# Kernel tuning notes

Hardware: AMD Instinct MI355X
Metric: run time of the kernel (lower is better)

The kernel has to match this reference:

```python
import jax, jax.numpy as jnp
import numpy as np

B = 1024          # batch
L = 200           # max_len (history length)
DIM = 64          # args.dim
ITEM_NUM = 100000 # vocab; table has ITEM_NUM+1 rows, row 0 = padding
NEG = -1e15       # mask additive constant used by the original module


def setup_inputs() -> dict:
    key = jax.random.key(0)
    k1, k2, k3, k4, k5 = jax.random.split(key, 5)
    log_seqs = jax.random.randint(k1, (B, L), 0, ITEM_NUM + 1)          # item ids, 0 = pad
    pred = jax.random.randint(k2, (B, 1), 0, ITEM_NUM + 1)              # gather targets
    item_emb = jax.random.normal(k3, (ITEM_NUM + 1, DIM), jnp.float32) * 0.02
    item_emb = item_emb.at[0].set(0.0)                                  # padding_idx=0
    attn_key = jax.random.uniform(k4, (1, DIM), jnp.float32)            # self.key (torch.rand init)
    pos_emb = jax.random.normal(k5, (L, DIM), jnp.float32) * 0.02       # positional table
    return {"log_seqs": log_seqs, "pred": pred, "item_emb": item_emb,
            "attn_key": attn_key, "pos_emb": pos_emb}


def reference(log_seqs, pred, item_emb, attn_key, pos_emb):
    dim = item_emb.shape[1]
    mask = log_seqs != 0                                  # [B, L] True where valid
    # log2feats (model='P2MAMO', dropout p=0 -> identity)
    seqs = item_emb[log_seqs] * jnp.sqrt(jnp.float32(dim))  # [B, L, D]
    seqs = seqs + pos_emb[None, :, :]
    seqs = seqs * mask[..., None]                         # zero out padded positions
    # single-query dot-product attention pooling with learned key
    sim = jnp.einsum('bld,d->bl', seqs, attn_key[0])      # (q*k).sum(-1)
    sim = sim + jnp.where(mask, 0.0, NEG)                 # sim + (~mask)*-1e15
    attn = jax.nn.softmax(sim, axis=-1)                   # [B, L]
    Q = jnp.einsum('bld,bl->bd', seqs, attn)              # [B, D]
    # training path (isEval=False): full-vocab logits -> softmax -> gather
    logits = Q @ item_emb.T                               # [B, V+1]
    probs = jax.nn.softmax(logits, axis=-1)
    pos_logits = jnp.take_along_axis(probs, pred, axis=1) # [B, 1]
    return pos_logits
```

## Files before the change

kernel.cpp:

```cpp
#include <hip/hip_runtime.h>
#include <math.h>

#define B_TOT   1024
#define L_SEQ   200
#define DIM     64
#define VOCAB   100001
#define NEG_BIG (-1e15f)
#define SEQ_STRIDE 68

typedef __bf16 bf16x8 __attribute__((ext_vector_type(8)));
typedef float  f32x4  __attribute__((ext_vector_type(4)));

__global__ __launch_bounds__(256) void pool_kernel(
    const int*   __restrict__ log_seqs,
    const float* __restrict__ item_emb,
    const float* __restrict__ attn_key,
    const float* __restrict__ pos_emb,
    float*       __restrict__ Q,
    __bf16*      __restrict__ Qb,
    __bf16*      __restrict__ Eb)
{
    const int b    = blockIdx.x;
    const int t    = threadIdx.x;
    const int wave = t >> 6;
    const int lane = t & 63;

    __shared__ float s_seq[L_SEQ][SEQ_STRIDE];
    __shared__ float s_attn[L_SEQ];
    __shared__ float s_red[4];
    __shared__ float s_q[4][DIM];

    {
        const long n8 = ((long)VOCAB * DIM) / 8;
        for (long g = (long)b * 256 + t; g < n8; g += (long)gridDim.x * 256) {
            const long i = g * 8;
            const float4 f0 = ((const float4*)(item_emb + i))[0];
            const float4 f1 = ((const float4*)(item_emb + i))[1];
            bf16x8 o;
            o[0] = (__bf16)f0.x; o[1] = (__bf16)f0.y; o[2] = (__bf16)f0.z; o[3] = (__bf16)f0.w;
            o[4] = (__bf16)f1.x; o[5] = (__bf16)f1.y; o[6] = (__bf16)f1.z; o[7] = (__bf16)f1.w;
            *(bf16x8*)(Eb + i) = o;
        }
    }

    float sim = -INFINITY;
    if (t < L_SEQ) {
        const int id = log_seqs[(long)b * L_SEQ + t];
        if (id == 0) {
            sim = NEG_BIG;
            #pragma unroll
            for (int i = 0; i < DIM / 4; ++i)
                *(float4*)(&s_seq[t][4 * i]) = make_float4(0.f, 0.f, 0.f, 0.f);
        } else {
            float acc = 0.f;
            const float4* e4 = (const float4*)(item_emb + (long)id * DIM);
            const float4* p4 = (const float4*)(pos_emb + t * DIM);
            #pragma unroll
            for (int i = 0; i < DIM / 4; ++i) {
                const float4 e = e4[i];
                const float4 p = p4[i];
                float4 f;
                f.x = fmaf(8.f, e.x, p.x);
                f.y = fmaf(8.f, e.y, p.y);
                f.z = fmaf(8.f, e.z, p.z);
                f.w = fmaf(8.f, e.w, p.w);
                *(float4*)(&s_seq[t][4 * i]) = f;
                acc += f.x * attn_key[4*i+0] + f.y * attn_key[4*i+1]
                     + f.z * attn_key[4*i+2] + f.w * attn_key[4*i+3];
            }
            sim = acc;
        }
    }

    float m = sim;
    #pragma unroll
    for (int off = 32; off > 0; off >>= 1) m = fmaxf(m, __shfl_xor(m, off));
    if (lane == 0) s_red[wave] = m;
    __syncthreads();
    m = fmaxf(fmaxf(s_red[0], s_red[1]), fmaxf(s_red[2], s_red[3]));
    __syncthreads();

    float p = (t < L_SEQ) ? __expf(sim - m) : 0.f;
    if (t < L_SEQ) s_attn[t] = p;
    float ls = p;
    #pragma unroll
    for (int off = 32; off > 0; off >>= 1) ls += __shfl_xor(ls, off);
    if (lane == 0) s_red[wave] = ls;
    __syncthreads();
    const float inv = 1.0f / (s_red[0] + s_red[1] + s_red[2] + s_red[3]);

    float q = 0.f;
    const int l0 = wave * (L_SEQ / 4);
    #pragma unroll 2
    for (int l = l0; l < l0 + (L_SEQ / 4); ++l)
        q = fmaf(s_attn[l], s_seq[l][lane], q);
    s_q[wave][lane] = q;
    __syncthreads();

    if (t < DIM) {
        const float qq = (s_q[0][t] + s_q[1][t] + s_q[2][t] + s_q[3][t]) * inv;
        Q[b * DIM + t]  = qq;
        Qb[b * DIM + t] = (__bf16)qq;
    }
}

#define NC        128
#define NBG       8
#define VT_TOTAL  6251
#define VT_FULL   6250

__global__ __launch_bounds__(256) void logits_mfma(
    const __bf16* __restrict__ Eb,
    const __bf16* __restrict__ Qb,
    float*        __restrict__ partials)
{
    const int bid   = blockIdx.x;
    const int xcd   = bid & 7;
    const int idx   = bid >> 3;
    const int chunk = xcd + 8 * (idx >> 3);
    const int bg    = idx & 7;
    const int wave  = threadIdx.x >> 6;
    const int lane  = threadIdx.x & 63;
    const int r16   = lane & 15;
    const int hi    = lane >> 4;

    __shared__ float s_part[4][128];

    bf16x8 a[8][2];
    #pragma unroll
    for (int t = 0; t < 8; ++t)
        #pragma unroll
        for (int s = 0; s < 2; ++s)
            a[t][s] = *(const bf16x8*)(Qb + ((bg*128 + t*16 + r16) * DIM) + s*32 + hi*8);

    const int per    = (VT_TOTAL + NC - 1) / NC;
    const int vt_end = min((chunk + 1) * per, VT_TOTAL);
    int vt = chunk * per + wave;

    float ssum[8][4];
    #pragma unroll
    for (int t = 0; t < 8; ++t)
        #pragma unroll
        for (int r = 0; r < 4; ++r) ssum[t][r] = 0.f;

    #define LOADB(dst0, dst1, vti) do {                                       \
        const int _row = min((vti) * 16 + r16, VOCAB - 1);                    \
        const __bf16* _p = Eb + (size_t)_row * DIM + hi * 8;                  \
        dst0 = *(const bf16x8*)_p;                                            \
        dst1 = *(const bf16x8*)(_p + 32);                                     \
    } while (0)

    bf16x8 b0, b1, d0, d1;
    LOADB(b0, b1, vt);
    LOADB(d0, d1, vt + 4);

    while (vt < vt_end) {
        const bf16x8 c00 = b0, c01 = b1, c10 = d0, c11 = d1;
        const int v0 = vt, v1 = vt + 4;
        vt += 8;
        LOADB(b0, b1, vt);
        LOADB(d0, d1, vt + 4);

        if (v0 < VT_FULL) {
            #pragma unroll
            for (int t = 0; t < 8; ++t) {
                f32x4 acc = {0.f, 0.f, 0.f, 0.f};
                acc = __builtin_amdgcn_mfma_f32_16x16x32_bf16(a[t][0], c00, acc, 0, 0, 0);
                acc = __builtin_amdgcn_mfma_f32_16x16x32_bf16(a[t][1], c01, acc, 0, 0, 0);
                #pragma unroll
                for (int r = 0; r < 4; ++r) ssum[t][r] += __expf(acc[r]);
            }
        } else {
            const bool valid = (v0 * 16 + r16) < VOCAB;
            #pragma unroll
            for (int t = 0; t < 8; ++t) {
                f32x4 acc = {0.f, 0.f, 0.f, 0.f};
                acc = __builtin_amdgcn_mfma_f32_16x16x32_bf16(a[t][0], c00, acc, 0, 0, 0);
                acc = __builtin_amdgcn_mfma_f32_16x16x32_bf16(a[t][1], c01, acc, 0, 0, 0);
                #pragma unroll
                for (int r = 0; r < 4; ++r) ssum[t][r] += valid ? __expf(acc[r]) : 0.f;
            }
        }
        if (v1 < vt_end) {
            if (v1 < VT_FULL) {
                #pragma unroll
                for (int t = 0; t < 8; ++t) {
                    f32x4 acc = {0.f, 0.f, 0.f, 0.f};
                    acc = __builtin_amdgcn_mfma_f32_16x16x32_bf16(a[t][0], c10, acc, 0, 0, 0);
                    acc = __builtin_amdgcn_mfma_f32_16x16x32_bf16(a[t][1], c11, acc, 0, 0, 0);
                    #pragma unroll
                    for (int r = 0; r < 4; ++r) ssum[t][r] += __expf(acc[r]);
                }
            } else {
                const bool valid = (v1 * 16 + r16) < VOCAB;
                #pragma unroll
                for (int t = 0; t < 8; ++t) {
                    f32x4 acc = {0.f, 0.f, 0.f, 0.f};
                    acc = __builtin_amdgcn_mfma_f32_16x16x32_bf16(a[t][0], c10, acc, 0, 0, 0);
                    acc = __builtin_amdgcn_mfma_f32_16x16x32_bf16(a[t][1], c11, acc, 0, 0, 0);
                    #pragma unroll
                    for (int r = 0; r < 4; ++r) ssum[t][r] += valid ? __expf(acc[r]) : 0.f;
                }
            }
        }
    }
    #undef LOADB

    #pragma unroll
    for (int t = 0; t < 8; ++t)
        #pragma unroll
        for (int r = 0; r < 4; ++r) {
            float v = ssum[t][r];
            v += __shfl_xor(v, 1);
            v += __shfl_xor(v, 2);
            v += __shfl_xor(v, 4);
            v += __shfl_xor(v, 8);
            ssum[t][r] = v;
        }

    if (r16 == 0) {
        #pragma unroll
        for (int t = 0; t < 8; ++t)
            #pragma unroll
            for (int r = 0; r < 4; ++r)
                s_part[wave][t * 16 + hi * 4 + r] = ssum[t][r];
    }
    __syncthreads();

    if (threadIdx.x < 128) {
        const int i = threadIdx.x;
        const float v = s_part[0][i] + s_part[1][i] + s_part[2][i] + s_part[3][i];
        partials[(size_t)chunk * B_TOT + bg * 128 + i] = v;
    }
}

__global__ __launch_bounds__(256) void finalize_kernel(
    const float* __restrict__ Q,
    const float* __restrict__ item_emb,
    const int*   __restrict__ pred,
    const float* __restrict__ partials,
    float*       __restrict__ out)
{
    const int b = blockIdx.x * 256 + threadIdx.x;

    float S = 0.f;
    for (int c = 0; c < NC; ++c)
        S += partials[(size_t)c * B_TOT + b];

    const int pv = pred[b];
    float acc = 0.f;
    const float4* e4 = (const float4*)(item_emb + (long)pv * DIM);
    const float4* q4 = (const float4*)(Q + b * DIM);
    #pragma unroll
    for (int i = 0; i < DIM / 4; ++i) {
        const float4 e = e4[i];
        const float4 q = q4[i];
        acc += e.x*q.x + e.y*q.y + e.z*q.z + e.w*q.w;
    }
    out[b] = __expf(acc) / S;
}

extern "C" void kernel_launch(void* const* d_in, const int* in_sizes, int n_in,
                              void* d_out, int out_size, void* d_ws, size_t ws_size,
                              hipStream_t stream)
{
    const int*   log_seqs = (const int*)  d_in[0];
    const int*   pred     = (const int*)  d_in[1];
    const float* item_emb = (const float*)d_in[2];
    const float* attn_key = (const float*)d_in[3];
    const float* pos_emb  = (const float*)d_in[4];
    float*       out      = (float*)d_out;

    char* ws = (char*)d_ws;
    __bf16* Eb       = (__bf16*)ws;
    __bf16* Qb       = (__bf16*)(ws + (size_t)VOCAB * DIM * 2);
    float*  Qf       = (float*) (ws + (size_t)VOCAB * DIM * 2 + (size_t)B_TOT * DIM * 2);
    float*  partials = (float*) ((char*)Qf + (size_t)B_TOT * DIM * 4);

    pool_kernel<<<B_TOT, 256, 0, stream>>>(log_seqs, item_emb, attn_key, pos_emb, Qf, Qb, Eb);
    logits_mfma<<<NBG * NC, 256, 0, stream>>>(Eb, Qb, partials);
    finalize_kernel<<<B_TOT / 256, 256, 0, stream>>>(Qf, item_emb, pred, partials, out);
}
```

Measured before the change: 68.60 us.

## Fold log2e into bf16 query, use exp2 in logits, bf16 LDS pooling

Pre-scales the bf16 query vector by log2(e) so the vocabulary softmax loop can call exp2f directly and skip the multiply inside __expf. Stores the pooled sequence in shared memory as bf16 instead of fp32, halving LDS use to allow more resident blocks. Moves the embedding-table bf16 conversion after the pooling work in the same kernel. Pooling precision drops to bf16, and any target-logit computation that reads Qb must account for the log2e scaling.

```diff
diff --git a/kernel.cpp b/kernel.cpp
--- a/kernel.cpp
+++ b/kernel.cpp
@@ -6,7 +6,8 @@
 #define DIM     64
 #define VOCAB   100001
 #define NEG_BIG (-1e15f)
-#define SEQ_STRIDE 68
+#define SEQ_ST16 66
+#define LOG2E   1.4426950408889634f
 
 typedef __bf16 bf16x8 __attribute__((ext_vector_type(8)));
 typedef float  f32x4  __attribute__((ext_vector_type(4)));
@@ -25,10 +26,81 @@
     const int wave = t >> 6;
     const int lane = t & 63;
 
-    __shared__ float s_seq[L_SEQ][SEQ_STRIDE];
+    __shared__ unsigned short s_seq16[L_SEQ][SEQ_ST16];
     __shared__ float s_attn[L_SEQ];
     __shared__ float s_red[4];
     __shared__ float s_q[4][DIM];
+
+    float sim = -INFINITY;
+    if (t < L_SEQ) {
+        const int id = log_seqs[(long)b * L_SEQ + t];
+        if (id == 0) {
+            sim = NEG_BIG;
+            const ushort2 z = make_ushort2(0, 0);
+            #pragma unroll
+            for (int i = 0; i < DIM / 2; ++i)
+                *(ushort2*)&s_seq16[t][2 * i] = z;
+        } else {
+            float acc = 0.f;
+            const float4* e4 = (const float4*)(item_emb + (long)id * DIM);
+            const float4* p4 = (const float4*)(pos_emb + t * DIM);
+            #pragma unroll
+            for (int i = 0; i < DIM / 4; ++i) {
+                const float4 e = e4[i];
+                const float4 p = p4[i];
+                float4 f;
+                f.x = fmaf(8.f, e.x, p.x);
+                f.y = fmaf(8.f, e.y, p.y);
+                f.z = fmaf(8.f, e.z, p.z);
+                f.w = fmaf(8.f, e.w, p.w);
+                const __bf16 h0 = (__bf16)f.x, h1 = (__bf16)f.y;
+                const __bf16 h2 = (__bf16)f.z, h3 = (__bf16)f.w;
+                ushort2 u0, u1;
+                u0.x = __builtin_bit_cast(unsigned short, h0);
+                u0.y = __builtin_bit_cast(unsigned short, h1);
+                u1.x = __builtin_bit_cast(unsigned short, h2);
+                u1.y = __builtin_bit_cast(unsigned short, h3);
+                *(ushort2*)&s_seq16[t][4 * i]     = u0;
+                *(ushort2*)&s_seq16[t][4 * i + 2] = u1;
+                acc += f.x * attn_key[4*i+0] + f.y * attn_key[4*i+1]
+                     + f.z * attn_key[4*i+2] + f.w * attn_key[4*i+3];
+            }
+            sim = acc;
+        }
+    }
+
+    float m = sim;
+    #pragma unroll
+    for (int off = 32; off > 0; off >>= 1) m = fmaxf(m, __shfl_xor(m, off));
+    if (lane == 0) s_red[wave] = m;
+    __syncthreads();
+    m = fmaxf(fmaxf(s_red[0], s_red[1]), fmaxf(s_red[2], s_red[3]));
+    __syncthreads();
+
+    float p = (t < L_SEQ) ? __expf(sim - m) : 0.f;
+    if (t < L_SEQ) s_attn[t] = p;
+    float ls = p;
+    #pragma unroll
+    for (int off = 32; off > 0; off >>= 1) ls += __shfl_xor(ls, off);
+    if (lane == 0) s_red[wave] = ls;
+    __syncthreads();
+    const float inv = 1.0f / (s_red[0] + s_red[1] + s_red[2] + s_red[3]);
+
+    float q = 0.f;
+    const int l0 = wave * (L_SEQ / 4);
+    #pragma unroll 2
+    for (int l = l0; l < l0 + (L_SEQ / 4); ++l) {
+        const unsigned int ui = (unsigned int)s_seq16[l][lane] << 16;
+        q = fmaf(s_attn[l], __builtin_bit_cast(float, ui), q);
+    }
+    s_q[wave][lane] = q;
+    __syncthreads();
+
+    if (t < DIM) {
+        const float qq = (s_q[0][t] + s_q[1][t] + s_q[2][t] + s_q[3][t]) * inv;
+        Q[b * DIM + t]  = qq;
+        Qb[b * DIM + t] = (__bf16)(qq * LOG2E);
+    }
 
     {
         const long n8 = ((long)VOCAB * DIM) / 8;
@@ -42,66 +114,6 @@
             *(bf16x8*)(Eb + i) = o;
         }
     }
-
-    float sim = -INFINITY;
-    if (t < L_SEQ) {
-        const int id = log_seqs[(long)b * L_SEQ + t];
-        if (id == 0) {
-            sim = NEG_BIG;
-            #pragma unroll
-            for (int i = 0; i < DIM / 4; ++i)
-                *(float4*)(&s_seq[t][4 * i]) = make_float4(0.f, 0.f, 0.f, 0.f);
-        } else {
-            float acc = 0.f;
-            const float4* e4 = (const float4*)(item_emb + (long)id * DIM);
-            const float4* p4 = (const float4*)(pos_emb + t * DIM);
-            #pragma unroll
-            for (int i = 0; i < DIM / 4; ++i) {
-                const float4 e = e4[i];
-                const float4 p = p4[i];
-                float4 f;
-                f.x = fmaf(8.f, e.x, p.x);
-                f.y = fmaf(8.f, e.y, p.y);
-                f.z = fmaf(8.f, e.z, p.z);
-                f.w = fmaf(8.f, e.w, p.w);
-                *(float4*)(&s_seq[t][4 * i]) = f;
-                acc += f.x * attn_key[4*i+0] + f.y * attn_key[4*i+1]
-                     + f.z * attn_key[4*i+2] + f.w * attn_key[4*i+3];
-            }
-            sim = acc;
-        }
-    }
-
-    float m = sim;
-    #pragma unroll
-    for (int off = 32; off > 0; off >>= 1) m = fmaxf(m, __shfl_xor(m, off));
-    if (lane == 0) s_red[wave] = m;
-    __syncthreads();
-    m = fmaxf(fmaxf(s_red[0], s_red[1]), fmaxf(s_red[2], s_red[3]));
-    __syncthreads();
-
-    float p = (t < L_SEQ) ? __expf(sim - m) : 0.f;
-    if (t < L_SEQ) s_attn[t] = p;
-    float ls = p;
-    #pragma unroll
-    for (int off = 32; off > 0; off >>= 1) ls += __shfl_xor(ls, off);
-    if (lane == 0) s_red[wave] = ls;
-    __syncthreads();
-    const float inv = 1.0f / (s_red[0] + s_red[1] + s_red[2] + s_red[3]);
-
-    float q = 0.f;
-    const int l0 = wave * (L_SEQ / 4);
-    #pragma unroll 2
-    for (int l = l0; l < l0 + (L_SEQ / 4); ++l)
-        q = fmaf(s_attn[l], s_seq[l][lane], q);
-    s_q[wave][lane] = q;
-    __syncthreads();
-
-    if (t < DIM) {
-        const float qq = (s_q[0][t] + s_q[1][t] + s_q[2][t] + s_q[3][t]) * inv;
-        Q[b * DIM + t]  = qq;
-        Qb[b * DIM + t] = (__bf16)qq;
-    }
 }
 
 #define NC        128
@@ -168,7 +180,7 @@
                 acc = __builtin_amdgcn_mfma_f32_16x16x32_bf16(a[t][0], c00, acc, 0, 0, 0);
                 acc = __builtin_amdgcn_mfma_f32_16x16x32_bf16(a[t][1], c01, acc, 0, 0, 0);
                 #pragma unroll
-                for (int r = 0; r < 4; ++r) ssum[t][r] += __expf(acc[r]);
+                for (int r = 0; r < 4; ++r) ssum[t][r] += exp2f(acc[r]);
             }
         } else {
             const bool valid = (v0 * 16 + r16) < VOCAB;
@@ -178,7 +190,7 @@
                 acc = __builtin_amdgcn_mfma_f32_16x16x32_bf16(a[t][0], c00, acc, 0, 0, 0);
                 acc = __builtin_amdgcn_mfma_f32_16x16x32_bf16(a[t][1], c01, acc, 0, 0, 0);
                 #pragma unroll
-                for (int r = 0; r < 4; ++r) ssum[t][r] += valid ? __expf(acc[r]) : 0.f;
+                for (int r = 0; r < 4; ++r) ssum[t][r] += valid ? exp2f(acc[r]) : 0.f;
             }
         }
         if (v1 < vt_end) {
@@ -189,7 +201,7 @@
                     acc = __builtin_amdgcn_mfma_f32_16x16x32_bf16(a[t][0], c10, acc, 0, 0, 0);
                     acc = __builtin_amdgcn_mfma_f32_16x16x32_bf16(a[t][1], c11, acc, 0, 0, 0);
                     #pragma unroll
-                    for (int r = 0; r < 4; ++r) ssum[t][r] += __expf(acc[r]);
+                    for (int r = 0; r < 4; ++r) ssum[t][r] += exp2f(acc[r]);
                 }
             } else {
                 const bool valid = (v1 * 16 + r16) < VOCAB;
@@ -199,7 +211,7 @@
                     acc = __builtin_amdgcn_mfma_f32_16x16x32_bf16(a[t][0], c10, acc, 0, 0, 0);
                     acc = __builtin_amdgcn_mfma_f32_16x16x32_bf16(a[t][1], c11, acc, 0, 0, 0);
                     #pragma unroll
-                    for (int r = 0; r < 4; ++r) ssum[t][r] += valid ? __expf(acc[r]) : 0.f;
+                    for (int r = 0; r < 4; ++r) ssum[t][r] += valid ? exp2f(acc[r]) : 0.f;
                 }
             }
         }
```

Measured after the change: 73.46 us. 1.07x slower.
